# Optimization experiments

Measured on AMD Instinct MI355X. Metric: run time of the kernel, lower is better.

The kernel has to match this reference:

```python
import jax, jax.numpy as jnp
import numpy as np

INPUT_DIM = 2048
NUM_EXPERTS = 64
TOP_K = 2


def setup_inputs() -> dict:
    key = jax.random.key(0)
    kx, kw, kb = jax.random.split(key, 3)
    x = jax.random.normal(kx, (4, 4096, INPUT_DIM), dtype=jnp.float32)
    # nn.Linear default init: U(-1/sqrt(fan_in), 1/sqrt(fan_in))
    bound = 1.0 / np.sqrt(INPUT_DIM)
    W = jax.random.uniform(kw, (INPUT_DIM, NUM_EXPERTS), dtype=jnp.float32, minval=-bound, maxval=bound)
    b = jax.random.uniform(kb, (NUM_EXPERTS,), dtype=jnp.float32, minval=-bound, maxval=bound)
    return {"x": x, "W": W, "b": b}


def reference(x, W, b):
    # router_logits = Linear(x); p = softmax(logits, -1); topk over experts
    logits = jnp.einsum("bsd,de->bse", x, W) + b          # [B, S, E]
    p = jax.nn.softmax(logits, axis=-1)                     # [B, S, E]
    gate_vals, expert_idx = jax.lax.top_k(p, TOP_K)         # [B, S, k] each
    return expert_idx, gate_vals
```

## Files before the change

### kernel.cpp

```cpp
#include <hip/hip_runtime.h>
#include <hip/hip_bf16.h>
#include <math.h>


#define DIM 2048
#define NE 64
#define RSTRIDE 2064

typedef __attribute__((ext_vector_type(8))) short short8;
typedef __attribute__((ext_vector_type(4))) float floatx4;

__device__ __forceinline__ short bf16bits(float v) {
  __hip_bfloat16 h = __float2bfloat16(v);
  return *(short*)&h;
}
__device__ __forceinline__ float bf16tof(short s) {
  union { unsigned int u; float f; } c;
  c.u = ((unsigned int)(unsigned short)s) << 16;
  return c.f;
}

__global__ void wprep_kernel(const float* __restrict__ W, short8* __restrict__ wf) {
  const int s = blockIdx.x >> 2, n = blockIdx.x & 3, l = threadIdx.x;
  const int d0 = s * 32 + (l >> 4) * 8;
  const int e = n * 16 + (l & 15);
  short8 vh, vl;
#pragma unroll
  for (int j = 0; j < 8; ++j) {
    float v = W[(size_t)(d0 + j) * NE + e];
    short h = bf16bits(v);
    vh[j] = h;
    vl[j] = bf16bits(v - bf16tof(h));
  }
  wf[(size_t)((s * 4 + n) * 2 + 0) * 64 + l] = vh;
  wf[(size_t)((s * 4 + n) * 2 + 1) * 64 + l] = vl;
}

__device__ __forceinline__ void async_copy16(const float* g, void* lds) {
  __builtin_amdgcn_global_load_lds(
      (const __attribute__((address_space(1))) unsigned int*)g,
      (__attribute__((address_space(3))) unsigned int*)lds, 16, 0, 0);
}

__global__ __launch_bounds__(256, 2) void router_gemm(
    const float* __restrict__ x, const short8* __restrict__ wf,
    float* __restrict__ part) {
  __shared__ alignas(16) char smem[32 * RSTRIDE];
  const int tid = threadIdx.x, lane = tid & 63, kq = tid >> 6;
  const int g = lane & 15, r4 = lane >> 4;
  const int gblk = blockIdx.x >> 2, s = blockIdx.x & 3;
  const int tok0 = gblk * 32;

  {
    const float* xb = x + (size_t)tok0 * DIM + s * 512;
#pragma unroll
    for (int r = 0; r < 8; ++r) {
      const int row = kq * 8 + r;
      const float* rp = xb + (size_t)row * DIM;
      char* dst = smem + row * RSTRIDE;
      async_copy16(rp + lane * 4, dst);
      async_copy16(rp + 256 + lane * 4, dst + 1024);
    }
  }

  floatx4 acc[2][4];
#pragma unroll
  for (int mt = 0; mt < 2; ++mt)
#pragma unroll
    for (int n = 0; n < 4; ++n) acc[mt][n] = (floatx4){0.f, 0.f, 0.f, 0.f};

  __syncthreads();

#pragma unroll
  for (int step = 0; step < 4; ++step) {
    const int sg = s * 16 + kq * 4 + step;
    const short8* wp = wf + (size_t)sg * 8 * 64;
    short8 Wh[4], Wl[4];
#pragma unroll
    for (int n = 0; n < 4; ++n) {
      Wh[n] = wp[(n * 2 + 0) * 64 + lane];
      Wl[n] = wp[(n * 2 + 1) * 64 + lane];
    }
    const int colb = kq * 512 + step * 128 + r4 * 32;
#pragma unroll
    for (int mt = 0; mt < 2; ++mt) {
      const int row = mt * 16 + g;
      const float* ap = (const float*)(smem + row * RSTRIDE + colb);
      floatx4 a0 = *(const floatx4*)ap;
      floatx4 a1 = *(const floatx4*)(ap + 4);
      short8 Ah, Al;
#pragma unroll
      for (int j = 0; j < 4; ++j) {
        short h = bf16bits(a0[j]);
        Ah[j] = h; Al[j] = bf16bits(a0[j] - bf16tof(h));
      }
#pragma unroll
      for (int j = 0; j < 4; ++j) {
        short h = bf16bits(a1[j]);
        Ah[4 + j] = h; Al[4 + j] = bf16bits(a1[j] - bf16tof(h));
      }
#pragma unroll
      for (int n = 0; n < 4; ++n) {
        acc[mt][n] = __builtin_amdgcn_mfma_f32_16x16x32_bf16(Ah, Wh[n], acc[mt][n], 0, 0, 0);
        acc[mt][n] = __builtin_amdgcn_mfma_f32_16x16x32_bf16(Ah, Wl[n], acc[mt][n], 0, 0, 0);
        acc[mt][n] = __builtin_amdgcn_mfma_f32_16x16x32_bf16(Al, Wh[n], acc[mt][n], 0, 0, 0);
      }
    }
  }

  __syncthreads();
  float* red = (float*)smem;
#pragma unroll
  for (int mt = 0; mt < 2; ++mt)
#pragma unroll
    for (int n = 0; n < 4; ++n)
#pragma unroll
      for (int r = 0; r < 4; ++r) {
        const int tokl = mt * 16 + r4 * 4 + r;
        const int e = n * 16 + g;
        red[(kq * 32 + tokl) * 65 + e] = acc[mt][n][r];
      }
  __syncthreads();

  float* pblk = part + (size_t)blockIdx.x * 2048;
#pragma unroll
  for (int i = tid; i < 512; i += 256) {
    const int f = i * 4, tok = f >> 6, e0 = f & 63;
    floatx4 v;
#pragma unroll
    for (int j = 0; j < 4; ++j)
      v[j] = red[(tok) * 65 + e0 + j] + red[(32 + tok) * 65 + e0 + j] +
             red[(64 + tok) * 65 + e0 + j] + red[(96 + tok) * 65 + e0 + j];
    *(floatx4*)(pblk + f) = v;
  }
}

__global__ __launch_bounds__(256) void router_topk(
    const float* __restrict__ part, const float* __restrict__ b,
    float* __restrict__ out, int ntok) {
  const int tid = threadIdx.x;
  const int T = blockIdx.x * 16 + (tid >> 4);
  const int eq = tid & 15, e0 = eq * 4;
  const float* pb = part + ((size_t)(T >> 5) * 4) * 2048 + (T & 31) * 64 + e0;
  floatx4 a = (floatx4){0.f, 0.f, 0.f, 0.f};
#pragma unroll
  for (int s = 0; s < 4; ++s) a += *(const floatx4*)(pb + (size_t)s * 2048);
  floatx4 bb = *(const floatx4*)(b + e0);
  float lv[4];
  float v1 = -INFINITY, v2 = -INFINITY;
  int i1 = 0, i2 = 0;
#pragma unroll
  for (int j = 0; j < 4; ++j) {
    float v = a[j] + bb[j];
    lv[j] = v;
    const int e = e0 + j;
    if (v > v1) { v2 = v1; i2 = i1; v1 = v; i1 = e; }
    else if (v > v2) { v2 = v; i2 = e; }
  }
#pragma unroll
  for (int off = 1; off < 16; off <<= 1) {
    float ov1 = __shfl_xor(v1, off, 64); int oi1 = __shfl_xor(i1, off, 64);
    float ov2 = __shfl_xor(v2, off, 64); int oi2 = __shfl_xor(i2, off, 64);
    bool aw = (v1 > ov1) || (v1 == ov1 && i1 < oi1);
    float nv1 = aw ? v1 : ov1; int ni1 = aw ? i1 : oi1;
    float c2v = aw ? ov1 : v1; int c2i = aw ? oi1 : i1;
    float w2v = aw ? v2 : ov2; int w2i = aw ? i2 : oi2;
    bool sw = (w2v > c2v) || (w2v == c2v && w2i < c2i);
    v2 = sw ? w2v : c2v; i2 = sw ? w2i : c2i;
    v1 = nv1; i1 = ni1;
  }
  float se = 0.f;
#pragma unroll
  for (int j = 0; j < 4; ++j) se += __expf(lv[j] - v1);
#pragma unroll
  for (int off = 1; off < 16; off <<= 1) se += __shfl_xor(se, off, 64);
  if (eq == 0) {
    out[T * 2 + 0] = (float)i1;
    out[T * 2 + 1] = (float)i2;
    out[ntok * 2 + T * 2 + 0] = 1.0f / se;
    out[ntok * 2 + T * 2 + 1] = __expf(v2 - v1) / se;
  }
}

extern "C" void kernel_launch(void* const* d_in, const int* in_sizes, int n_in,
                              void* d_out, int out_size, void* d_ws, size_t ws_size,
                              hipStream_t stream) {
  const float* x = (const float*)d_in[0];
  const float* W = (const float*)d_in[1];
  const float* b = (const float*)d_in[2];
  float* out = (float*)d_out;
  const int ntok = in_sizes[0] / DIM;
  short8* wf = (short8*)d_ws;
  float* part = (float*)((char*)d_ws + 512 * 1024);

  wprep_kernel<<<256, 64, 0, stream>>>(W, wf);
  router_gemm<<<(ntok / 32) * 4, 256, 0, stream>>>(x, wf, part);
  router_topk<<<ntok / 16, 256, 0, stream>>>(part, b, out, ntok);
}
```

Measured before the change: 206.8 us.

## Halve token tile to 16 rows per block and use register-staged loads

The GEMM block tile shrinks from 32 to 16 tokens, which halves LDS use and raises the occupancy hint from 2 to 4 blocks per CU. The grid doubles in size. The async global-to-LDS copies are replaced by vectorized loads into registers followed by LDS stores, and the partial-sum layout and the top-k indexing are adjusted to match. The trade-off is that each block loads its W fragments from global memory for only 16 tokens instead of 32, so weight reuse per load is halved.

```diff
diff --git a/kernel.cpp b/kernel.cpp
--- a/kernel.cpp
+++ b/kernel.cpp
@@ -5,7 +5,7 @@
 
 #define DIM 2048
 #define NE 64
-#define RSTRIDE 2064
+#define TSTRIDE 2064
 
 typedef __attribute__((ext_vector_type(8))) short short8;
 typedef __attribute__((ext_vector_type(4))) float floatx4;
@@ -36,102 +36,84 @@
   wf[(size_t)((s * 4 + n) * 2 + 1) * 64 + l] = vl;
 }
 
-__device__ __forceinline__ void async_copy16(const float* g, void* lds) {
-  __builtin_amdgcn_global_load_lds(
-      (const __attribute__((address_space(1))) unsigned int*)g,
-      (__attribute__((address_space(3))) unsigned int*)lds, 16, 0, 0);
-}
-
-__global__ __launch_bounds__(256, 2) void router_gemm(
+__global__ __launch_bounds__(256, 4) void router_gemm(
     const float* __restrict__ x, const short8* __restrict__ wf,
     float* __restrict__ part) {
-  __shared__ alignas(16) char smem[32 * RSTRIDE];
+  __shared__ alignas(16) char smem[16 * TSTRIDE];
   const int tid = threadIdx.x, lane = tid & 63, kq = tid >> 6;
   const int g = lane & 15, r4 = lane >> 4;
   const int gblk = blockIdx.x >> 2, s = blockIdx.x & 3;
-  const int tok0 = gblk * 32;
+  const int tok0 = gblk * 16;
 
   {
-    const float* xb = x + (size_t)tok0 * DIM + s * 512;
+    const int row = kq * 4 + r4;
+    const float* rp = x + (size_t)(tok0 + row) * DIM + s * 512 + g * 4;
+    char* wb = smem + row * TSTRIDE + g * 16;
+    float4 t[8];
 #pragma unroll
-    for (int r = 0; r < 8; ++r) {
-      const int row = kq * 8 + r;
-      const float* rp = xb + (size_t)row * DIM;
-      char* dst = smem + row * RSTRIDE;
-      async_copy16(rp + lane * 4, dst);
-      async_copy16(rp + 256 + lane * 4, dst + 1024);
-    }
+    for (int p = 0; p < 8; ++p) t[p] = *(const float4*)(rp + p * 64);
+#pragma unroll
+    for (int p = 0; p < 8; ++p) *(float4*)(wb + p * 256) = t[p];
   }
 
-  floatx4 acc[2][4];
+  floatx4 acc[4];
 #pragma unroll
-  for (int mt = 0; mt < 2; ++mt)
-#pragma unroll
-    for (int n = 0; n < 4; ++n) acc[mt][n] = (floatx4){0.f, 0.f, 0.f, 0.f};
+  for (int n = 0; n < 4; ++n) acc[n] = (floatx4){0.f, 0.f, 0.f, 0.f};
 
   __syncthreads();
 
 #pragma unroll
   for (int step = 0; step < 4; ++step) {
     const int sg = s * 16 + kq * 4 + step;
-    const short8* wp = wf + (size_t)sg * 8 * 64;
+    const short8* wp = wf + (size_t)sg * 512;
     short8 Wh[4], Wl[4];
 #pragma unroll
     for (int n = 0; n < 4; ++n) {
       Wh[n] = wp[(n * 2 + 0) * 64 + lane];
       Wl[n] = wp[(n * 2 + 1) * 64 + lane];
     }
-    const int colb = kq * 512 + step * 128 + r4 * 32;
+    const char* ap = smem + g * TSTRIDE + kq * 512 + step * 128 + r4 * 32;
+    floatx4 a0 = *(const floatx4*)ap;
+    floatx4 a1 = *(const floatx4*)(ap + 16);
+    short8 Ah, Al;
 #pragma unroll
-    for (int mt = 0; mt < 2; ++mt) {
-      const int row = mt * 16 + g;
-      const float* ap = (const float*)(smem + row * RSTRIDE + colb);
-      floatx4 a0 = *(const floatx4*)ap;
-      floatx4 a1 = *(const floatx4*)(ap + 4);
-      short8 Ah, Al;
+    for (int j = 0; j < 4; ++j) {
+      short h = bf16bits(a0[j]);
+      Ah[j] = h; Al[j] = bf16bits(a0[j] - bf16tof(h));
+    }
 #pragma unroll
-      for (int j = 0; j < 4; ++j) {
-        short h = bf16bits(a0[j]);
-        Ah[j] = h; Al[j] = bf16bits(a0[j] - bf16tof(h));
-      }
+    for (int j = 0; j < 4; ++j) {
+      short h = bf16bits(a1[j]);
+      Ah[4 + j] = h; Al[4 + j] = bf16bits(a1[j] - bf16tof(h));
+    }
 #pragma unroll
-      for (int j = 0; j < 4; ++j) {
-        short h = bf16bits(a1[j]);
-        Ah[4 + j] = h; Al[4 + j] = bf16bits(a1[j] - bf16tof(h));
-      }
-#pragma unroll
-      for (int n = 0; n < 4; ++n) {
-        acc[mt][n] = __builtin_amdgcn_mfma_f32_16x16x32_bf16(Ah, Wh[n], acc[mt][n], 0, 0, 0);
-        acc[mt][n] = __builtin_amdgcn_mfma_f32_16x16x32_bf16(Ah, Wl[n], acc[mt][n], 0, 0, 0);
-        acc[mt][n] = __builtin_amdgcn_mfma_f32_16x16x32_bf16(Al, Wh[n], acc[mt][n], 0, 0, 0);
-      }
+    for (int n = 0; n < 4; ++n) {
+      acc[n] = __builtin_amdgcn_mfma_f32_16x16x32_bf16(Ah, Wh[n], acc[n], 0, 0, 0);
+      acc[n] = __builtin_amdgcn_mfma_f32_16x16x32_bf16(Ah, Wl[n], acc[n], 0, 0, 0);
+      acc[n] = __builtin_amdgcn_mfma_f32_16x16x32_bf16(Al, Wh[n], acc[n], 0, 0, 0);
     }
   }
 
   __syncthreads();
   float* red = (float*)smem;
 #pragma unroll
-  for (int mt = 0; mt < 2; ++mt)
+  for (int n = 0; n < 4; ++n)
 #pragma unroll
-    for (int n = 0; n < 4; ++n)
-#pragma unroll
-      for (int r = 0; r < 4; ++r) {
-        const int tokl = mt * 16 + r4 * 4 + r;
-        const int e = n * 16 + g;
-        red[(kq * 32 + tokl) * 65 + e] = acc[mt][n][r];
-      }
+    for (int r = 0; r < 4; ++r) {
+      const int tokl = r4 * 4 + r;
+      const int e = n * 16 + g;
+      red[(kq * 16 + tokl) * 65 + e] = acc[n][r];
+    }
   __syncthreads();
 
-  float* pblk = part + (size_t)blockIdx.x * 2048;
+  {
+    const int tok = tid >> 4, e0 = (tid & 15) * 4;
+    floatx4 v = (floatx4){0.f, 0.f, 0.f, 0.f};
 #pragma unroll
-  for (int i = tid; i < 512; i += 256) {
-    const int f = i * 4, tok = f >> 6, e0 = f & 63;
-    floatx4 v;
+    for (int k4 = 0; k4 < 4; ++k4)
 #pragma unroll
-    for (int j = 0; j < 4; ++j)
-      v[j] = red[(tok) * 65 + e0 + j] + red[(32 + tok) * 65 + e0 + j] +
-             red[(64 + tok) * 65 + e0 + j] + red[(96 + tok) * 65 + e0 + j];
-    *(floatx4*)(pblk + f) = v;
+      for (int j = 0; j < 4; ++j) v[j] += red[(k4 * 16 + tok) * 65 + e0 + j];
+    *(floatx4*)(part + (size_t)blockIdx.x * 1024 + tok * 64 + e0) = v;
   }
 }
 
@@ -141,10 +123,10 @@
   const int tid = threadIdx.x;
   const int T = blockIdx.x * 16 + (tid >> 4);
   const int eq = tid & 15, e0 = eq * 4;
-  const float* pb = part + ((size_t)(T >> 5) * 4) * 2048 + (T & 31) * 64 + e0;
+  const float* pb = part + (size_t)((T >> 4) * 4) * 1024 + (T & 15) * 64 + e0;
   floatx4 a = (floatx4){0.f, 0.f, 0.f, 0.f};
 #pragma unroll
-  for (int s = 0; s < 4; ++s) a += *(const floatx4*)(pb + (size_t)s * 2048);
+  for (int s = 0; s < 4; ++s) a += *(const floatx4*)(pb + (size_t)s * 1024);
   floatx4 bb = *(const floatx4*)(b + e0);
   float lv[4];
   float v1 = -INFINITY, v2 = -INFINITY;
@@ -194,6 +176,6 @@
   float* part = (float*)((char*)d_ws + 512 * 1024);
 
   wprep_kernel<<<256, 64, 0, stream>>>(W, wf);
-  router_gemm<<<(ntok / 32) * 4, 256, 0, stream>>>(x, wf, part);
+  router_gemm<<<(ntok / 16) * 4, 256, 0, stream>>>(x, wf, part);
   router_topk<<<ntok / 16, 256, 0, stream>>>(part, b, out, ntok);
 }
```

New measurement: 200.2 us. -3.2%, faster.
